# Kernel tuning notes

Hardware: AMD Instinct MI355X
Metric: run time of the kernel (lower is better)

## Reference

```python
import jax, jax.numpy as jnp
import numpy as np

LN_EPS = 1e-12


def setup_inputs() -> dict:
    key = jax.random.key(0)
    k1, k2, k3, k4 = jax.random.split(key, 4)
    B, H, L, D = 2, 12, 2048, 64
    q = jax.random.normal(k1, (B, H, L, D), dtype=jnp.float32)
    k = jax.random.normal(k2, (B, H, L, D), dtype=jnp.float32)
    v = jax.random.normal(k3, (B, H, L, D), dtype=jnp.float32)
    mask = jax.random.randint(k4, (1, 1, L, L), 0, 2).astype(jnp.int32)
    gamma = jnp.ones((D,), dtype=jnp.float32)
    beta = jnp.zeros((D,), dtype=jnp.float32)
    return {"q": q, "k": k, "v": v, "mask": mask, "gamma": gamma, "beta": beta}


def reference(q, k, v, mask, gamma, beta):
    # score = q @ k^T  -> [B, H, L, L]
    score = jnp.einsum("bhqd,bhkd->bhqk", q, k)
    # masked_fill(mask == 0, -10000)
    score = jnp.where(mask == 0, jnp.float32(-10000.0), score)
    # result = score @ v -> [B, H, L, D]  (no softmax)
    result = jnp.einsum("bhqk,bhkd->bhqd", score, v)
    # layer norm over the last dim (d_tensor)
    mean = jnp.mean(result, axis=-1, keepdims=True)
    var = jnp.var(result, axis=-1, keepdims=True)
    normed = (result - mean) / jnp.sqrt(var + LN_EPS)
    return normed * gamma + beta
```

## Files before the change

### kernel.cpp

```cpp
#include <hip/hip_runtime.h>

#define SEQ 2048
#define HD 64
#define NBH 24
#define ROWB 144

#define MB_OFF   0
#define MB_BYTES (32 * 32 * 512)
#define QB_OFF   (MB_OFF + MB_BYTES)
#define QK_BYTES (NBH * SEQ * HD * 2)
#define KB_OFF   (QB_OFF + QK_BYTES)
#define VT_OFF   (KB_OFF + QK_BYTES)
#define WS_NEED  ((size_t)(VT_OFF + QK_BYTES))

typedef __bf16 bfrag8 __attribute__((ext_vector_type(8)));
typedef __bf16 bf16x4 __attribute__((ext_vector_type(4)));
typedef float  floatx4 __attribute__((ext_vector_type(4)));

__device__ __forceinline__ floatx4 mfma_16x16x32(bfrag8 a, bfrag8 b, floatx4 c) {
    return __builtin_amdgcn_mfma_f32_16x16x32_bf16(a, b, c, 0, 0, 0);
}

__global__ __launch_bounds__(256)
void prep_kernel(const float* __restrict__ qp, const float* __restrict__ kp,
                 const float* __restrict__ vp, const int* __restrict__ maskp,
                 unsigned char* __restrict__ ws)
{
    __shared__ __attribute__((aligned(16))) unsigned char parena[64 * 68 * 4];
    const int t = threadIdx.x;
    const int b = blockIdx.x;

    if (b < 1536) {
        int gt  = b * 256 + t;
        int row = gt >> 3;
        int c   = gt & 7;
        const floatx4* qs = (const floatx4*)(qp + row * 64 + c * 8);
        const floatx4* ks = (const floatx4*)(kp + row * 64 + c * 8);
        floatx4 q0 = qs[0], q1 = qs[1];
        floatx4 k0 = ks[0], k1 = ks[1];
        bfrag8 qpk, kpk;
        #pragma unroll
        for (int i = 0; i < 4; ++i) {
            qpk[i] = (__bf16)q0[i]; qpk[4 + i] = (__bf16)q1[i];
            kpk[i] = (__bf16)k0[i]; kpk[4 + i] = (__bf16)k1[i];
        }
        *(bfrag8*)(ws + QB_OFF + row * 128 + c * 16) = qpk;
        *(bfrag8*)(ws + KB_OFF + row * 128 + c * 16) = kpk;
    } else if (b < 2304) {
        int bb = b - 1536, bh = bb >> 5, kt = bb & 31;
        float* lf = (float*)parena;
        const floatx4* vg = (const floatx4*)(vp + (bh * SEQ + kt * 64) * 64);
        #pragma unroll
        for (int it = 0; it < 4; ++it) {
            int f = t + it * 256;
            int r = f >> 4, c4 = f & 15;
            floatx4 val = vg[f];
            #pragma unroll
            for (int i = 0; i < 4; ++i) lf[r * 68 + c4 * 4 + i] = val[i];
        }
        __syncthreads();
        int d = t >> 2, kseg = t & 3;
        unsigned char* tb = ws + VT_OFF + (size_t)(bh * 32 + kt) * 8192 + d * 128;
        #pragma unroll
        for (int jj = 0; jj < 2; ++jj) {
            bfrag8 pk;
            #pragma unroll
            for (int e = 0; e < 8; ++e)
                pk[e] = (__bf16)lf[(kseg * 16 + jj * 8 + e) * 68 + d];
            *(bfrag8*)(tb + (kseg * 2 + jj) * 16) = pk;
        }
    } else {
        int cc = b - 2304, qtb = cc >> 5, kt = cc & 31;
        const int w = t >> 6, lane = t & 63;
        #pragma unroll
        for (int it = 0; it < 16; ++it) {
            int rr = it * 4 + w;
            unsigned long long bl = __ballot(maskp[(qtb * 64 + rr) * SEQ + kt * 64 + lane] != 0);
            if (lane == 0)
                *(unsigned long long*)(ws + MB_OFF + (size_t)((qtb * 32 + kt) * 64 + rr) * 8) = bl;
        }
    }
}

__global__ __launch_bounds__(256, 3)
void normattn_main(const unsigned char* __restrict__ ws,
                   const float* __restrict__ gammap, const float* __restrict__ betap,
                   float* __restrict__ outp)
{
    __shared__ __attribute__((aligned(16))) unsigned char sK[2][64 * ROWB];
    __shared__ __attribute__((aligned(16))) unsigned char sV[2][64 * ROWB];
    __shared__ __attribute__((aligned(16))) unsigned char sS[2][64 * 128];

    const int tid  = threadIdx.x;
    const int w    = tid >> 6;
    const int lane = tid & 63;
    const int quad = lane >> 4;
    const int l16  = lane & 15;
    const int qtb  = blockIdx.x;
    const int bh   = blockIdx.y;
    const int q0   = qtb * 64;
    const int swz  = l16 & 7;

    const unsigned char* gKb = ws + KB_OFF + (size_t)(bh * SEQ) * 128;
    const unsigned char* gVb = ws + VT_OFF + (size_t)(bh * 32) * 8192;
    const unsigned char* gMb = ws + MB_OFF + (size_t)(qtb * 32) * 512;

    bfrag8 qb[4][2];
    #pragma unroll
    for (int qt = 0; qt < 4; ++qt) {
        const unsigned char* gQ = ws + QB_OFF + (size_t)(bh * SEQ + q0 + qt * 16 + l16) * 128 + quad * 16;
        qb[qt][0] = *(const bfrag8*)gQ;
        qb[qt][1] = *(const bfrag8*)(gQ + 64);
    }

    floatx4 acc[4];
    #pragma unroll
    for (int i = 0; i < 4; ++i) acc[i] = (floatx4)0.0f;
    const int qrow_loc = w * 16 + quad * 4;

    const int sr0 = tid >> 3, sc0 = tid & 7;
    const int sr1 = (tid + 256) >> 3, sc1 = tid & 7;

    auto load_tile = [&](int kt, bfrag8 (&kr)[2], bfrag8 (&vr)[2]) {
        const unsigned char* gK = gKb + (size_t)kt * 8192;
        const unsigned char* gV = gVb + (size_t)kt * 8192;
        kr[0] = *(const bfrag8*)(gK + tid * 16);
        kr[1] = *(const bfrag8*)(gK + (tid + 256) * 16);
        vr[0] = *(const bfrag8*)(gV + tid * 16);
        vr[1] = *(const bfrag8*)(gV + (tid + 256) * 16);
    };
    auto write_tile = [&](int s, bfrag8 (&kr)[2], bfrag8 (&vr)[2]) {
        *(bfrag8*)(&sK[s][0] + sr0 * ROWB + sc0 * 16) = kr[0];
        *(bfrag8*)(&sK[s][0] + sr1 * ROWB + sc1 * 16) = kr[1];
        *(bfrag8*)(&sV[s][0] + sr0 * ROWB + sc0 * 16) = vr[0];
        *(bfrag8*)(&sV[s][0] + sr1 * ROWB + sc1 * 16) = vr[1];
    };

    auto qk_phase = [&](int tt, const unsigned char* cK, const unsigned long long (&mr)[4]) {
        bfrag8 ka0 = *(const bfrag8*)(cK + (w * 16 + l16) * ROWB + quad * 16);
        bfrag8 ka1 = *(const bfrag8*)(cK + (w * 16 + l16) * ROWB + 64 + quad * 16);
        #pragma unroll
        for (int qt = 0; qt < 4; ++qt) {
            floatx4 st = (floatx4)0.0f;
            st = mfma_16x16x32(ka0, qb[qt][0], st);
            st = mfma_16x16x32(ka1, qb[qt][1], st);
            unsigned long long m4 = mr[qt] >> (w * 16 + quad * 4);
            bf16x4 pk;
            #pragma unroll
            for (int r = 0; r < 4; ++r) {
                float v = ((m4 >> r) & 1ull) ? st[r] : -10000.0f;
                pk[r] = (__bf16)v;
            }
            *(bf16x4*)(&sS[tt][0] + (qt * 16 + l16) * 128 +
                       (((w * 2 + (quad >> 1)) ^ swz) * 16) + (quad & 1) * 8) = pk;
        }
    };
    auto pv_phase = [&](int tt, const unsigned char* cV) {
        #pragma unroll
        for (int kc2 = 0; kc2 < 2; ++kc2) {
            bfrag8 pa = *(const bfrag8*)(&sS[tt][0] + (w * 16 + l16) * 128 +
                                         (((kc2 * 4 + quad) ^ swz) * 16));
            #pragma unroll
            for (int nt = 0; nt < 4; ++nt) {
                bfrag8 vb = *(const bfrag8*)(cV + (nt * 16 + l16) * ROWB + kc2 * 64 + quad * 16);
                acc[nt] = mfma_16x16x32(pa, vb, acc[nt]);
            }
        }
    };

    {
        bfrag8 k0r[2], v0r[2], k1r[2], v1r[2];
        load_tile(0, k0r, v0r);
        load_tile(1, k1r, v1r);
        write_tile(0, k0r, v0r);
        write_tile(1, k1r, v1r);
    }
    asm volatile("s_waitcnt lgkmcnt(0)" ::: "memory");
    asm volatile("s_barrier" ::: "memory");

    for (int i = 0; i < 16; ++i) {
        const int t0 = 2 * i, t1 = 2 * i + 1;

        bfrag8 kA[2], vA[2];
        if (i < 15) load_tile(t0 + 2, kA, vA);

        unsigned long long mr0[4], mr1[4];
        #pragma unroll
        for (int qt = 0; qt < 4; ++qt) {
            mr0[qt] = *(const unsigned long long*)(gMb + (size_t)t0 * 512 + (qt * 16 + l16) * 8);
            mr1[qt] = *(const unsigned long long*)(gMb + (size_t)t1 * 512 + (qt * 16 + l16) * 8);
        }

        qk_phase(0, &sK[0][0], mr0);
        qk_phase(1, &sK[1][0], mr1);
        asm volatile("s_waitcnt lgkmcnt(0)" ::: "memory");
        asm volatile("s_barrier" ::: "memory");

        bfrag8 kB[2], vB[2];
        if (i < 15) load_tile(t0 + 3, kB, vB);

        pv_phase(0, &sV[0][0]);
        pv_phase(1, &sV[1][0]);
        asm volatile("s_waitcnt lgkmcnt(0)" ::: "memory");
        asm volatile("s_barrier" ::: "memory");

        if (i < 15) {
            write_tile(0, kA, vA);
            write_tile(1, kB, vB);
        }
        asm volatile("s_waitcnt lgkmcnt(0)" ::: "memory");
        asm volatile("s_barrier" ::: "memory");
    }

    float g[4], bt[4];
    #pragma unroll
    for (int nt = 0; nt < 4; ++nt) {
        g[nt]  = gammap[nt * 16 + l16];
        bt[nt] = betap[nt * 16 + l16];
    }
    #pragma unroll
    for (int r = 0; r < 4; ++r) {
        float s = 0.0f, s2 = 0.0f;
        #pragma unroll
        for (int nt = 0; nt < 4; ++nt) { float x = acc[nt][r]; s += x; s2 += x * x; }
        #pragma unroll
        for (int off = 1; off < 16; off <<= 1) {
            s  += __shfl_xor(s, off);
            s2 += __shfl_xor(s2, off);
        }
        float mean = s * (1.0f / 64.0f);
        float var  = s2 * (1.0f / 64.0f) - mean * mean;
        float rstd = rsqrtf(var + 1e-12f);
        float* orow = outp + (size_t)(bh * SEQ + q0 + qrow_loc + r) * 64;
        #pragma unroll
        for (int nt = 0; nt < 4; ++nt)
            orow[nt * 16 + l16] = (acc[nt][r] - mean) * rstd * g[nt] + bt[nt];
    }
}

#define KROW 72
#define SROW 40
__global__ __launch_bounds__(256, 4)
void normattn_fallback(const float* __restrict__ qp, const float* __restrict__ kp,
                       const float* __restrict__ vp, const int* __restrict__ maskp,
                       const float* __restrict__ gammap, const float* __restrict__ betap,
                       float* __restrict__ outp)
{
    __shared__ __attribute__((aligned(16))) __bf16 sQ[64 * KROW];
    __shared__ __attribute__((aligned(16))) __bf16 sK[64 * KROW];
    __shared__ __attribute__((aligned(16))) __bf16 sV[64 * KROW];
    __shared__ __attribute__((aligned(16))) __bf16 sS[4][16 * SROW];
    __shared__ __attribute__((aligned(8)))  unsigned int sMw[64][2];

    const int tid = threadIdx.x, wave = tid >> 6, lane = tid & 63;
    const int quad = lane >> 4, l16 = lane & 15;
    const int q0 = blockIdx.x * 64, bh = blockIdx.y;
    const int base = bh * SEQ * HD;
    {
        const floatx4* qg = (const floatx4*)(qp + base + q0 * HD);
        #pragma unroll
        for (int it = 0; it < 4; ++it) {
            int idx = tid + it * 256, r = idx >> 4, c = idx & 15;
            floatx4 val = qg[idx];
            bf16x4 pk = {(__bf16)val[0], (__bf16)val[1], (__bf16)val[2], (__bf16)val[3]};
            *(bf16x4*)&sQ[r * KROW + c * 4] = pk;
        }
    }
    __syncthreads();
    bfrag8 qa0 = *(const bfrag8*)&sQ[(wave * 16 + l16) * KROW + quad * 8];
    bfrag8 qa1 = *(const bfrag8*)&sQ[(wave * 16 + l16) * KROW + quad * 8 + 32];
    floatx4 acc[4];
    #pragma unroll
    for (int i = 0; i < 4; ++i) acc[i] = (floatx4)0.0f;
    const int qrow_loc = wave * 16 + quad * 4;
    const int qrb = q0 + qrow_loc;
    for (int kb = 0; kb < SEQ; kb += 64) {
        __syncthreads();
        {
            const floatx4* kg = (const floatx4*)(kp + base + kb * HD);
            #pragma unroll
            for (int it = 0; it < 4; ++it) {
                int idx = tid + it * 256, r = idx >> 4, c = idx & 15;
                floatx4 val = kg[idx];
                bf16x4 pk = {(__bf16)val[0], (__bf16)val[1], (__bf16)val[2], (__bf16)val[3]};
                *(bf16x4*)&sK[r * KROW + c * 4] = pk;
            }
        }
        {
            int d = tid & 63;
            #pragma unroll
            for (int it = 0; it < 4; ++it) {
                int k4 = (tid >> 6) + it * 4;
                bf16x4 pk;
                #pragma unroll
                for (int i = 0; i < 4; ++i) pk[i] = (__bf16)vp[base + (kb + k4 * 4 + i) * HD + d];
                *(bf16x4*)&sV[d * KROW + k4 * 4] = pk;
            }
        }
        #pragma unroll
        for (int it = 0; it < 16; ++it) {
            int rr = it * 4 + wave;
            unsigned long long bl = __ballot(maskp[(q0 + rr) * SEQ + kb + lane] != 0);
            if (lane == 0) { sMw[rr][0] = (unsigned)bl; sMw[rr][1] = (unsigned)(bl >> 32); }
        }
        __syncthreads();
        unsigned long long mrow[4];
        #pragma unroll
        for (int r = 0; r < 4; ++r) mrow[r] = *(const unsigned long long*)&sMw[qrow_loc + r][0];
        #pragma unroll
        for (int kc = 0; kc < 64; kc += 32) {
            floatx4 s0 = (floatx4)0.0f, s1 = (floatx4)0.0f;
            bfrag8 b00 = *(const bfrag8*)&sK[(kc + l16) * KROW + quad * 8];
            bfrag8 b01 = *(const bfrag8*)&sK[(kc + l16) * KROW + quad * 8 + 32];
            bfrag8 b10 = *(const bfrag8*)&sK[(kc + 16 + l16) * KROW + quad * 8];
            bfrag8 b11 = *(const bfrag8*)&sK[(kc + 16 + l16) * KROW + quad * 8 + 32];
            s0 = mfma_16x16x32(qa0, b00, s0);
            s0 = mfma_16x16x32(qa1, b01, s0);
            s1 = mfma_16x16x32(qa0, b10, s1);
            s1 = mfma_16x16x32(qa1, b11, s1);
            #pragma unroll
            for (int r = 0; r < 4; ++r) {
                float v0 = ((mrow[r] >> (kc + l16)) & 1ull) ? s0[r] : -10000.0f;
                float v1 = ((mrow[r] >> (kc + 16 + l16)) & 1ull) ? s1[r] : -10000.0f;
                sS[wave][(quad * 4 + r) * SROW + l16] = (__bf16)v0;
                sS[wave][(quad * 4 + r) * SROW + 16 + l16] = (__bf16)v1;
            }
            asm volatile("s_waitcnt lgkmcnt(0)" ::: "memory");
            bfrag8 pa = *(const bfrag8*)&sS[wave][l16 * SROW + quad * 8];
            #pragma unroll
            for (int nt = 0; nt < 4; ++nt) {
                bfrag8 vb = *(const bfrag8*)&sV[(nt * 16 + l16) * KROW + kc + quad * 8];
                acc[nt] = mfma_16x16x32(pa, vb, acc[nt]);
            }
        }
    }
    float g[4], bt[4];
    #pragma unroll
    for (int nt = 0; nt < 4; ++nt) { g[nt] = gammap[nt * 16 + l16]; bt[nt] = betap[nt * 16 + l16]; }
    #pragma unroll
    for (int r = 0; r < 4; ++r) {
        float s = 0.0f, s2 = 0.0f;
        #pragma unroll
        for (int nt = 0; nt < 4; ++nt) { float xx = acc[nt][r]; s += xx; s2 += xx * xx; }
        #pragma unroll
        for (int off = 1; off < 16; off <<= 1) { s += __shfl_xor(s, off); s2 += __shfl_xor(s2, off); }
        float mean = s * (1.0f / 64.0f);
        float var = s2 * (1.0f / 64.0f) - mean * mean;
        float rstd = rsqrtf(var + 1e-12f);
        float* orow = outp + base + (qrb + r) * HD;
        #pragma unroll
        for (int nt = 0; nt < 4; ++nt)
            orow[nt * 16 + l16] = (acc[nt][r] - mean) * rstd * g[nt] + bt[nt];
    }
}

extern "C" void kernel_launch(void* const* d_in, const int* in_sizes, int n_in,
                              void* d_out, int out_size, void* d_ws, size_t ws_size,
                              hipStream_t stream) {
    const float* q     = (const float*)d_in[0];
    const float* k     = (const float*)d_in[1];
    const float* v     = (const float*)d_in[2];
    const int*   mask  = (const int*)d_in[3];
    const float* gamma = (const float*)d_in[4];
    const float* beta  = (const float*)d_in[5];
    float* out = (float*)d_out;

    dim3 grid(32, NBH);
    if (ws_size >= WS_NEED) {
        unsigned char* ws = (unsigned char*)d_ws;
        prep_kernel<<<3328, 256, 0, stream>>>(q, k, v, mask, ws);
        normattn_main<<<grid, 256, 0, stream>>>(ws, gamma, beta, out);
    } else {
        normattn_fallback<<<grid, 256, 0, stream>>>(q, k, v, mask, gamma, beta, out);
    }
}
```

Baseline: 147.7 us.

## Load K fragments directly from global into registers, drop K shared tile

```diff
diff --git a/kernel.cpp b/kernel.cpp
--- a/kernel.cpp
+++ b/kernel.cpp
@@ -87,7 +87,6 @@
                    const float* __restrict__ gammap, const float* __restrict__ betap,
                    float* __restrict__ outp)
 {
-    __shared__ __attribute__((aligned(16))) unsigned char sK[2][64 * ROWB];
     __shared__ __attribute__((aligned(16))) unsigned char sV[2][64 * ROWB];
     __shared__ __attribute__((aligned(16))) unsigned char sS[2][64 * 128];
 
@@ -121,24 +120,27 @@
     const int sr0 = tid >> 3, sc0 = tid & 7;
     const int sr1 = (tid + 256) >> 3, sc1 = tid & 7;
 
-    auto load_tile = [&](int kt, bfrag8 (&kr)[2], bfrag8 (&vr)[2]) {
-        const unsigned char* gK = gKb + (size_t)kt * 8192;
+    auto load_vtile = [&](int kt, bfrag8 (&vr)[2]) {
         const unsigned char* gV = gVb + (size_t)kt * 8192;
-        kr[0] = *(const bfrag8*)(gK + tid * 16);
-        kr[1] = *(const bfrag8*)(gK + (tid + 256) * 16);
         vr[0] = *(const bfrag8*)(gV + tid * 16);
         vr[1] = *(const bfrag8*)(gV + (tid + 256) * 16);
     };
-    auto write_tile = [&](int s, bfrag8 (&kr)[2], bfrag8 (&vr)[2]) {
-        *(bfrag8*)(&sK[s][0] + sr0 * ROWB + sc0 * 16) = kr[0];
-        *(bfrag8*)(&sK[s][0] + sr1 * ROWB + sc1 * 16) = kr[1];
+    auto write_vtile = [&](int s, bfrag8 (&vr)[2]) {
         *(bfrag8*)(&sV[s][0] + sr0 * ROWB + sc0 * 16) = vr[0];
         *(bfrag8*)(&sV[s][0] + sr1 * ROWB + sc1 * 16) = vr[1];
     };
-
-    auto qk_phase = [&](int tt, const unsigned char* cK, const unsigned long long (&mr)[4]) {
-        bfrag8 ka0 = *(const bfrag8*)(cK + (w * 16 + l16) * ROWB + quad * 16);
-        bfrag8 ka1 = *(const bfrag8*)(cK + (w * 16 + l16) * ROWB + 64 + quad * 16);
+    auto load_ka = [&](int kt, bfrag8& a0, bfrag8& a1) {
+        const unsigned char* gK = gKb + (size_t)kt * 8192 + (w * 16 + l16) * 128 + quad * 16;
+        a0 = *(const bfrag8*)gK;
+        a1 = *(const bfrag8*)(gK + 64);
+    };
+    auto load_mr = [&](int kt, unsigned long long (&m)[4]) {
+        #pragma unroll
+        for (int qt = 0; qt < 4; ++qt)
+            m[qt] = *(const unsigned long long*)(gMb + (size_t)kt * 512 + (qt * 16 + l16) * 8);
+    };
+
+    auto qk_phase = [&](int tt, bfrag8 ka0, bfrag8 ka1, const unsigned long long (&mr)[4]) {
         #pragma unroll
         for (int qt = 0; qt < 4; ++qt) {
             floatx4 st = (floatx4)0.0f;
@@ -168,36 +170,40 @@
         }
     };
 
+    bfrag8 ka00, ka01, ka10, ka11;
+    unsigned long long mr0[4], mr1[4];
     {
-        bfrag8 k0r[2], v0r[2], k1r[2], v1r[2];
-        load_tile(0, k0r, v0r);
-        load_tile(1, k1r, v1r);
-        write_tile(0, k0r, v0r);
-        write_tile(1, k1r, v1r);
+        bfrag8 v0r[2], v1r[2];
+        load_vtile(0, v0r);
+        load_vtile(1, v1r);
+        load_ka(0, ka00, ka01);
+        load_ka(1, ka10, ka11);
+        load_mr(0, mr0);
+        load_mr(1, mr1);
+        write_vtile(0, v0r);
+        write_vtile(1, v1r);
     }
     asm volatile("s_waitcnt lgkmcnt(0)" ::: "memory");
     asm volatile("s_barrier" ::: "memory");
 
     for (int i = 0; i < 16; ++i) {
-        const int t0 = 2 * i, t1 = 2 * i + 1;
-
-        bfrag8 kA[2], vA[2];
-        if (i < 15) load_tile(t0 + 2, kA, vA);
-
-        unsigned long long mr0[4], mr1[4];
-        #pragma unroll
-        for (int qt = 0; qt < 4; ++qt) {
-            mr0[qt] = *(const unsigned long long*)(gMb + (size_t)t0 * 512 + (qt * 16 + l16) * 8);
-            mr1[qt] = *(const unsigned long long*)(gMb + (size_t)t1 * 512 + (qt * 16 + l16) * 8);
-        }
-
-        qk_phase(0, &sK[0][0], mr0);
-        qk_phase(1, &sK[1][0], mr1);
+        const int t0 = 2 * i;
+
+        bfrag8 vA[2], vB[2];
+        if (i < 15) load_vtile(t0 + 2, vA);
+
+        qk_phase(0, ka00, ka01, mr0);
+        qk_phase(1, ka10, ka11, mr1);
         asm volatile("s_waitcnt lgkmcnt(0)" ::: "memory");
         asm volatile("s_barrier" ::: "memory");
 
-        bfrag8 kB[2], vB[2];
-        if (i < 15) load_tile(t0 + 3, kB, vB);
+        if (i < 15) {
+            load_vtile(t0 + 3, vB);
+            load_ka(t0 + 2, ka00, ka01);
+            load_ka(t0 + 3, ka10, ka11);
+            load_mr(t0 + 2, mr0);
+            load_mr(t0 + 3, mr1);
+        }
 
         pv_phase(0, &sV[0][0]);
         pv_phase(1, &sV[1][0]);
@@ -205,8 +211,8 @@
         asm volatile("s_barrier" ::: "memory");
 
         if (i < 15) {
-            write_tile(0, kA, vA);
-            write_tile(1, kB, vB);
+            write_vtile(0, vA);
+            write_vtile(1, vB);
         }
         asm volatile("s_waitcnt lgkmcnt(0)" ::: "memory");
         asm volatile("s_barrier" ::: "memory");
```

Measured after the change: 151.5 us. +2.6%, slower.
